# Performance work log

Measured on AMD Instinct MI355X. Metric: run time of the kernel, lower is better.

## Reference

```python
import jax, jax.numpy as jnp
import numpy as np

N, C, H, W, G = 8, 256, 128, 128, 32
STRIDE = 8


def setup_inputs() -> dict:
    key = jax.random.key(0)
    kx, kxy, kwh = jax.random.split(key, 3)
    x = jax.random.normal(kx, (N, C, H, W), dtype=jnp.float32)
    # valid pixel-space boxes: x1,y1 in [0, 900), w,h in [16, 200)
    xy1 = jax.random.uniform(kxy, (N, G, 2), minval=0.0, maxval=900.0)
    wh = jax.random.uniform(kwh, (N, G, 2), minval=16.0, maxval=200.0)
    xy2 = jnp.clip(xy1 + wh, 0.0, STRIDE * W - 1.0)
    gt_bboxes = jnp.concatenate([xy1, xy2], axis=-1).astype(jnp.float32)  # [N,G,4] (x1,y1,x2,y2)
    return {"x": x, "gt_bboxes": gt_bboxes, "stride": STRIDE, "epoch": 5}


def reference(x, gt_bboxes, stride, epoch):
    # x: [N,C,H,W]; gt_bboxes: [N,G,4] pixel coords (x1,y1,x2,y2)
    n, c, h, w = x.shape
    b = gt_bboxes / stride
    x1 = jnp.floor(b[..., 0])  # [N,G]
    y1 = jnp.floor(b[..., 1])
    x2 = jnp.ceil(b[..., 2])
    y2 = jnp.ceil(b[..., 3])
    ys = jnp.arange(h, dtype=b.dtype)
    xs = jnp.arange(w, dtype=b.dtype)
    # inside tests, vectorized over all boxes (replaces per-bbox slice assignment)
    in_y = (ys[None, None, :] >= y1[..., None]) & (ys[None, None, :] < y2[..., None])  # [N,G,H]
    in_x = (xs[None, None, :] >= x1[..., None]) & (xs[None, None, :] < x2[..., None])  # [N,G,W]
    mask = jnp.any(in_y[:, :, :, None] & in_x[:, :, None, :], axis=1)  # [N,H,W], union of boxes
    mask = mask.astype(x.dtype)
    # channel-mean of masked (detached) features, scaled by cosine schedule
    e = jnp.mean(jax.lax.stop_gradient(x) * mask[:, None, :, :], axis=1, keepdims=True)  # [N,1,H,W]
    alpha = 0.5 * (1.0 + jnp.cos(jnp.pi * epoch / 22.0))
    excitations = jax.lax.stop_gradient(e * alpha)
    return x + excitations  # broadcast over channel dim
```

## Files before the change

### kernel.cpp

```cpp
#include <hip/hip_runtime.h>
#include <math.h>

constexpr int N_ = 8, C_ = 256, H_ = 128, W_ = 128, G_ = 32;
constexpr int HW  = H_ * W_;
constexpr int CHW = C_ * HW;
constexpr int T4   = 16;
constexpr int TPIX = 64;

__global__ __launch_bounds__(512) void fused_exc_kernel(
    const float* __restrict__ x, const float* __restrict__ bb,
    const int* __restrict__ stride_p, const int* __restrict__ epoch_p,
    float* __restrict__ out)
{
    __shared__ float4 xs[C_][T4];
    __shared__ float4 psum[32][T4];
    __shared__ float4 bbx[G_];
    __shared__ float  e_lds[TPIX];

    int bid  = blockIdx.x;
    int n    = bid >> 8;
    int rem  = bid & 255;
    int row  = rem >> 1;
    int half = rem & 1;

    int tid = threadIdx.x;
    int c0  = tid >> 4;
    int q   = tid & 15;

    if (tid < G_) bbx[tid] = reinterpret_cast<const float4*>(bb)[n * G_ + tid];

    size_t goff = (size_t)n * CHW + (size_t)c0 * HW + (size_t)row * W_ + half * TPIX + q * 4;
    const float* xp = x + goff;

    float4 s = make_float4(0.f, 0.f, 0.f, 0.f);
    #pragma unroll
    for (int k = 0; k < 8; ++k) {
        float4 v = *reinterpret_cast<const float4*>(xp + (size_t)(32 * k) * HW);
        xs[c0 + 32 * k][q] = v;
        s.x += v.x; s.y += v.y; s.z += v.z; s.w += v.w;
    }
    psum[c0][q] = s;
    __syncthreads();

    #pragma unroll
    for (int off = 16; off >= 1; off >>= 1) {
        if (tid < off * 16) {
            float4 a = psum[c0][q];
            float4 b = psum[c0 + off][q];
            psum[c0][q] = make_float4(a.x + b.x, a.y + b.y, a.z + b.z, a.w + b.w);
        }
        __syncthreads();
    }

    if (tid < TPIX) {
        float inv   = 1.0f / (float)(*stride_p);
        float alpha = 0.5f * (1.0f + cosf((float)M_PI * (float)(*epoch_p) / 22.0f));
        float scale = alpha / (float)C_;
        float hf = (float)row;
        float wf = (float)(half * TPIX + tid);
        bool m = false;
        for (int g = 0; g < G_; ++g) {
            float4 bv = bbx[g];
            float x1 = floorf(bv.x * inv), y1 = floorf(bv.y * inv);
            float x2 = ceilf (bv.z * inv), y2 = ceilf (bv.w * inv);
            m = m || (hf >= y1 && hf < y2 && wf >= x1 && wf < x2);
        }
        float sum = reinterpret_cast<float*>(&psum[0][0])[tid];
        e_lds[tid] = m ? sum * scale : 0.0f;
    }
    __syncthreads();

    float4 e4 = reinterpret_cast<float4*>(e_lds)[q];
    float* op = out + goff;
    #pragma unroll
    for (int k = 0; k < 8; ++k) {
        float4 v = xs[c0 + 32 * k][q];
        *reinterpret_cast<float4*>(op + (size_t)(32 * k) * HW) =
            make_float4(v.x + e4.x, v.y + e4.y, v.z + e4.z, v.w + e4.w);
    }
}

extern "C" void kernel_launch(void* const* d_in, const int* in_sizes, int n_in,
                              void* d_out, int out_size, void* d_ws, size_t ws_size,
                              hipStream_t stream) {
    const float* x  = (const float*)d_in[0];
    const float* bb = (const float*)d_in[1];
    const int* stride_p = (const int*)d_in[2];
    const int* epoch_p  = (const int*)d_in[3];
    float* out = (float*)d_out;

    int grid = N_ * H_ * 2;
    fused_exc_kernel<<<grid, 512, 0, stream>>>(x, bb, stride_p, epoch_p, out);
}
```

Before: 52.04 us.

## Keep tile in registers and reduce channels with wave shuffles

The 64KB LDS staging buffer for the channel tile is removed, and each thread keeps its eight float4 values in registers until the write-back. The channel sum now uses cross-lane xor shuffles inside each wave plus one LDS exchange of eight partial sums, replacing a five-step shared-memory tree with a barrier after each step. Every thread computes the box mask for its own four pixels redundantly, which removes the final barrier and the LDS broadcast of the excitation values. Freeing the LDS should let more blocks fit per CU, at the cost of higher register use and duplicated mask work across threads.

```diff
diff --git a/kernel.cpp b/kernel.cpp
--- a/kernel.cpp
+++ b/kernel.cpp
@@ -4,7 +4,6 @@
 constexpr int N_ = 8, C_ = 256, H_ = 128, W_ = 128, G_ = 32;
 constexpr int HW  = H_ * W_;
 constexpr int CHW = C_ * HW;
-constexpr int T4   = 16;
 constexpr int TPIX = 64;
 
 __global__ __launch_bounds__(512) void fused_exc_kernel(
@@ -12,10 +11,8 @@
     const int* __restrict__ stride_p, const int* __restrict__ epoch_p,
     float* __restrict__ out)
 {
-    __shared__ float4 xs[C_][T4];
-    __shared__ float4 psum[32][T4];
+    __shared__ float4 psum[8][16];
     __shared__ float4 bbx[G_];
-    __shared__ float  e_lds[TPIX];
 
     int bid  = blockIdx.x;
     int n    = bid >> 8;
@@ -23,60 +20,68 @@
     int row  = rem >> 1;
     int half = rem & 1;
 
-    int tid = threadIdx.x;
-    int c0  = tid >> 4;
-    int q   = tid & 15;
+    int tid  = threadIdx.x;
+    int wv   = tid >> 6;
+    int lane = tid & 63;
+    int c0   = tid >> 4;
+    int q    = tid & 15;
 
     if (tid < G_) bbx[tid] = reinterpret_cast<const float4*>(bb)[n * G_ + tid];
 
     size_t goff = (size_t)n * CHW + (size_t)c0 * HW + (size_t)row * W_ + half * TPIX + q * 4;
     const float* xp = x + goff;
 
+    float4 v[8];
     float4 s = make_float4(0.f, 0.f, 0.f, 0.f);
     #pragma unroll
     for (int k = 0; k < 8; ++k) {
-        float4 v = *reinterpret_cast<const float4*>(xp + (size_t)(32 * k) * HW);
-        xs[c0 + 32 * k][q] = v;
-        s.x += v.x; s.y += v.y; s.z += v.z; s.w += v.w;
+        v[k] = *reinterpret_cast<const float4*>(xp + (size_t)(32 * k) * HW);
+        s.x += v[k].x; s.y += v[k].y; s.z += v[k].z; s.w += v[k].w;
     }
-    psum[c0][q] = s;
+    s.x += __shfl_xor(s.x, 16); s.y += __shfl_xor(s.y, 16);
+    s.z += __shfl_xor(s.z, 16); s.w += __shfl_xor(s.w, 16);
+    s.x += __shfl_xor(s.x, 32); s.y += __shfl_xor(s.y, 32);
+    s.z += __shfl_xor(s.z, 32); s.w += __shfl_xor(s.w, 32);
+    if (lane < 16) psum[wv][q] = s;
     __syncthreads();
 
+    float4 sum = psum[0][q];
     #pragma unroll
-    for (int off = 16; off >= 1; off >>= 1) {
-        if (tid < off * 16) {
-            float4 a = psum[c0][q];
-            float4 b = psum[c0 + off][q];
-            psum[c0][q] = make_float4(a.x + b.x, a.y + b.y, a.z + b.z, a.w + b.w);
-        }
-        __syncthreads();
+    for (int w = 1; w < 8; ++w) {
+        float4 p = psum[w][q];
+        sum.x += p.x; sum.y += p.y; sum.z += p.z; sum.w += p.w;
     }
 
-    if (tid < TPIX) {
-        float inv   = 1.0f / (float)(*stride_p);
-        float alpha = 0.5f * (1.0f + cosf((float)M_PI * (float)(*epoch_p) / 22.0f));
-        float scale = alpha / (float)C_;
-        float hf = (float)row;
-        float wf = (float)(half * TPIX + tid);
-        bool m = false;
-        for (int g = 0; g < G_; ++g) {
-            float4 bv = bbx[g];
-            float x1 = floorf(bv.x * inv), y1 = floorf(bv.y * inv);
-            float x2 = ceilf (bv.z * inv), y2 = ceilf (bv.w * inv);
-            m = m || (hf >= y1 && hf < y2 && wf >= x1 && wf < x2);
+    float inv   = 1.0f / (float)(*stride_p);
+    float alpha = 0.5f * (1.0f + cosf((float)M_PI * (float)(*epoch_p) / 22.0f));
+    float scale = alpha / (float)C_;
+
+    float hf = (float)row;
+    float w0 = (float)(half * TPIX + q * 4);
+    int m = 0;
+    for (int g = 0; g < G_; ++g) {
+        float4 bv = bbx[g];
+        float x1 = floorf(bv.x * inv), y1 = floorf(bv.y * inv);
+        float x2 = ceilf (bv.z * inv), y2 = ceilf (bv.w * inv);
+        if (hf >= y1 && hf < y2) {
+            #pragma unroll
+            for (int j = 0; j < 4; ++j) {
+                float wf = w0 + (float)j;
+                if (wf >= x1 && wf < x2) m |= 1 << j;
+            }
         }
-        float sum = reinterpret_cast<float*>(&psum[0][0])[tid];
-        e_lds[tid] = m ? sum * scale : 0.0f;
     }
-    __syncthreads();
+    float4 e4;
+    e4.x = (m & 1) ? sum.x * scale : 0.f;
+    e4.y = (m & 2) ? sum.y * scale : 0.f;
+    e4.z = (m & 4) ? sum.z * scale : 0.f;
+    e4.w = (m & 8) ? sum.w * scale : 0.f;
 
-    float4 e4 = reinterpret_cast<float4*>(e_lds)[q];
     float* op = out + goff;
     #pragma unroll
     for (int k = 0; k < 8; ++k) {
-        float4 v = xs[c0 + 32 * k][q];
         *reinterpret_cast<float4*>(op + (size_t)(32 * k) * HW) =
-            make_float4(v.x + e4.x, v.y + e4.y, v.z + e4.z, v.w + e4.w);
+            make_float4(v[k].x + e4.x, v[k].y + e4.y, v[k].z + e4.z, v[k].w + e4.w);
     }
 }
 
```

Result: faster. 48.58 us (-6.6%).
